# Kernel tuning notes

Hardware: AMD Instinct MI355X
Metric: run time of the kernel (lower is better)

The kernel has to match this reference:

```python
import jax, jax.numpy as jnp
import numpy as np
from jax import lax

PAD = 2          # shift_size // 2
SHIFT = 5        # shift_size


def _soft_shift(fp, gw, gb, axis):
    """fp: padded feature map [B,C,Hp,Wp]; gw: [S,C] 1x1-conv weight; gb: [S].
    Gated soft-shift along `axis` (2=H, 3=W), then crop padding."""
    logits = jnp.einsum('bchw,sc->bshw', fp, gw) + gb[None, :, None, None]
    w = jax.nn.softmax(logits, axis=1)  # [B,S,Hp,Wp]
    acc = jnp.zeros_like(fp)
    for i, s in enumerate(range(-PAD, PAD + 1)):
        acc = acc + jnp.roll(fp, s, axis=axis) * w[:, i:i + 1]
    return acc[:, :, PAD:-PAD, PAD:-PAD]


def _dwconv(x, w, b):
    # x: [B,C,H,W], w: [C,1,3,3] depthwise, b: [C]
    y = lax.conv_general_dilated(x, w, window_strides=(1, 1), padding='SAME',
                                 dimension_numbers=('NCHW', 'OIHW', 'NCHW'),
                                 feature_group_count=x.shape[1])
    return y + b[None, :, None, None]


def setup_inputs() -> dict:
    key = jax.random.key(0)
    ks = jax.random.split(key, 12)
    B, H, W = 16, 128, 128
    C, Ch = 96, 384
    x = jax.random.normal(ks[0], (B, H * W, C), dtype=jnp.float32)
    fc1_w = jax.random.normal(ks[1], (C, Ch), dtype=jnp.float32) * 0.02
    fc1_b = jnp.zeros((Ch,), dtype=jnp.float32)
    dw_w = jax.random.normal(ks[2], (Ch, 1, 3, 3), dtype=jnp.float32) * np.sqrt(2.0 / 9.0)
    dw_b = jnp.zeros((Ch,), dtype=jnp.float32)
    fc2_w = jax.random.normal(ks[3], (Ch, C), dtype=jnp.float32) * 0.02
    fc2_b = jnp.zeros((C,), dtype=jnp.float32)
    gh_w = jax.random.normal(ks[4], (SHIFT, C), dtype=jnp.float32) * np.sqrt(2.0 / SHIFT)
    gh_b = jnp.zeros((SHIFT,), dtype=jnp.float32)
    gw_w = jax.random.normal(ks[5], (SHIFT, Ch), dtype=jnp.float32) * np.sqrt(2.0 / SHIFT)
    gw_b = jnp.zeros((SHIFT,), dtype=jnp.float32)
    return {"x": x, "H": H, "W": W,
            "fc1_w": fc1_w, "fc1_b": fc1_b, "dw_w": dw_w, "dw_b": dw_b,
            "fc2_w": fc2_w, "fc2_b": fc2_b,
            "gh_w": gh_w, "gh_b": gh_b, "gw_w": gw_w, "gw_b": gw_b}


def reference(x, H, W, fc1_w, fc1_b, dw_w, dw_b, fc2_w, fc2_b, gh_w, gh_b, gw_w, gw_b):
    B, N, C = x.shape
    # soft-shift along H on input channels
    fmap = jnp.transpose(x, (0, 2, 1)).reshape(B, C, H, W)
    fmap_p = jnp.pad(fmap, ((0, 0), (0, 0), (PAD, PAD), (PAD, PAD)))
    mixed_h = _soft_shift(fmap_p, gh_w, gh_b, axis=2)          # [B,C,H,W]
    tokens = jnp.transpose(mixed_h.reshape(B, C, H * W), (0, 2, 1))
    tokens = tokens @ fc1_w + fc1_b                            # [B,N,Ch]
    Ch = tokens.shape[-1]
    t = jnp.transpose(tokens, (0, 2, 1)).reshape(B, Ch, H, W)
    t = _dwconv(t, dw_w, dw_b)
    tokens = jnp.transpose(t.reshape(B, Ch, H * W), (0, 2, 1))
    tokens = jax.nn.gelu(tokens, approximate=False)
    # soft-shift along W on hidden channels
    fmap2 = jnp.transpose(tokens, (0, 2, 1)).reshape(B, Ch, H, W)
    fmap2_p = jnp.pad(fmap2, ((0, 0), (0, 0), (PAD, PAD), (PAD, PAD)))
    mixed_w = _soft_shift(fmap2_p, gw_w, gw_b, axis=3)         # [B,Ch,H,W]
    tokens2 = jnp.transpose(mixed_w.reshape(B, Ch, H * W), (0, 2, 1))
    return tokens2 @ fc2_w + fc2_b                             # [B,N,C_out]
```

## Files before the change

kernel.cpp:

```cpp
#include <hip/hip_runtime.h>
#include <cstddef>

#define Cc 96
#define CH 384
#define Mtok 262144
#define Mi   16384

typedef unsigned short us8 __attribute__((ext_vector_type(8)));
typedef float f8 __attribute__((ext_vector_type(8)));
typedef short s8v __attribute__((ext_vector_type(8)));
typedef float f4v __attribute__((ext_vector_type(4)));

static __device__ __forceinline__ float b2f(unsigned short s){
  union { unsigned u; float f; } v; v.u = ((unsigned)s) << 16; return v.f;
}
static __device__ __forceinline__ unsigned short f2b(float f){
  union { float f; unsigned u; } v; v.f = f;
  unsigned r = v.u + 0x7fffu + ((v.u >> 16) & 1u);
  return (unsigned short)(r >> 16);
}

__global__ __launch_bounds__(64) void k_wprep(const float* __restrict__ dww,
    float* __restrict__ wt_t){
  int i = blockIdx.x*64 + threadIdx.x;
  if (i < 9*CH){
    int tap = i / CH, c = i - tap*CH;
    wt_t[i] = dww[c*9 + tap];
  }
}

__global__ __launch_bounds__(256) void k_wprep2(const float* __restrict__ fc2w,
    unsigned short* __restrict__ Bp){
  int i = blockIdx.x*256 + threadIdx.x;
  int j = i & 7;
  int t = i >> 3;
  int l = t & 63;
  int u = t >> 6;
  int ks = u % 12, nt = u / 12;
  int k   = ks*32 + (l>>4)*8 + j;
  int col = nt*16 + (l&15);
  Bp[i] = f2b(fc2w[(size_t)k*96 + col]);
}

__global__ __launch_bounds__(256) void k_wprep1(const float* __restrict__ fc1w,
    unsigned short* __restrict__ Bp1){
  int i = blockIdx.x*256 + threadIdx.x;
  int j = i & 7;
  int t = i >> 3;
  int l = t & 63;
  int u = t >> 6;
  int ks = u % 3, nt = u / 3;
  int k   = ks*32 + (l>>4)*8 + j;
  int col = nt*16 + (l&15);
  Bp1[i] = f2b(fc1w[(size_t)k*CH + col]);
}

__global__ __launch_bounds__(320) void k_fc1f(const float* __restrict__ x,
    const float* __restrict__ gh_w, const float* __restrict__ gh_b,
    const unsigned short* __restrict__ Bp1, const float* __restrict__ fc1b,
    unsigned short* __restrict__ hid, int base, int Mloc){
  __shared__ unsigned short A[80][100];
  __shared__ unsigned short Y[80][104];
  __shared__ float wh_s[80][5];
  const int tid = threadIdx.x;
  const int bid = (int)blockIdx.x;
  const int img  = bid >> 8;
  const int rem  = bid & 255;
  const int band = rem >> 5;
  const int colg = rem & 31;
  const int h0 = band*16;
  const int w0 = colg*4;
  const size_t lbase = (size_t)img*16384;

  {
    const int sr = tid>>2, sq = tid&3;
    const int r = sr>>2, cw = sr&3;
    const int h = h0 + r - 2;
    const bool valid = ((unsigned)h < 128u);
    float part[5] = {0.f,0.f,0.f,0.f,0.f};
    if (valid){
      const float* src = &x[((size_t)base + lbase + h*128 + w0 + cw)*Cc + sq*24];
      #pragma unroll
      for (int p=0;p<3;++p){
        float4 v0 = *(const float4*)&src[p*8];
        float4 v1 = *(const float4*)&src[p*8+4];
        us8 ov;
        ov[0]=f2b(v0.x); ov[1]=f2b(v0.y); ov[2]=f2b(v0.z); ov[3]=f2b(v0.w);
        ov[4]=f2b(v1.x); ov[5]=f2b(v1.y); ov[6]=f2b(v1.z); ov[7]=f2b(v1.w);
        *(us8*)&A[sr][sq*24 + p*8] = ov;
        #pragma unroll
        for (int s=0;s<5;++s){
          float4 g0 = *(const float4*)&gh_w[s*Cc + sq*24 + p*8];
          float4 g1 = *(const float4*)&gh_w[s*Cc + sq*24 + p*8 + 4];
          part[s]=fmaf(v0.x,g0.x,part[s]); part[s]=fmaf(v0.y,g0.y,part[s]);
          part[s]=fmaf(v0.z,g0.z,part[s]); part[s]=fmaf(v0.w,g0.w,part[s]);
          part[s]=fmaf(v1.x,g1.x,part[s]); part[s]=fmaf(v1.y,g1.y,part[s]);
          part[s]=fmaf(v1.z,g1.z,part[s]); part[s]=fmaf(v1.w,g1.w,part[s]);
        }
      }
    } else {
      us8 z = {0,0,0,0,0,0,0,0};
      #pragma unroll
      for (int p=0;p<3;++p) *(us8*)&A[sr][sq*24 + p*8] = z;
    }
    #pragma unroll
    for (int s=0;s<5;++s){
      float v = part[s];
      v += __shfl_xor(v, 1, 64);
      v += __shfl_xor(v, 2, 64);
      part[s] = v;
    }
    if (sq==0 && valid){
      float l[5];
      #pragma unroll
      for (int s=0;s<5;++s) l[s] = part[s] + gh_b[s];
      float mx = fmaxf(fmaxf(fmaxf(l[0],l[1]),fmaxf(l[2],l[3])),l[4]);
      float sum=0.f;
      #pragma unroll
      for (int s=0;s<5;++s){ l[s]=__expf(l[s]-mx); sum+=l[s]; }
      float inv=1.f/sum;
      #pragma unroll
      for (int s=0;s<5;++s) wh_s[sr][s] = l[s]*inv;
    }
  }
  __syncthreads();

  const int wv = tid>>6, l = tid&63;
  const int row16 = l&15, g = l>>4;
  const int tl = tid>>2, q = tid&3;
  const int it = (2 + (tl>>2))*4 + (tl&3);
  const int hh = h0 + (tl>>2);
  float swgt[5];
  unsigned short* o = nullptr;
  if (tid < 256){
    #pragma unroll
    for (int i=0;i<5;++i){
      int h2 = hh - (i-2);
      swgt[i] = ((unsigned)h2 < 128u) ? wh_s[it][i] : 0.f;
    }
    o = &hid[(lbase + hh*128 + w0 + (tl&3))*CH];
  }

  #pragma unroll 1
  for (int chunk=0;chunk<4;++chunk){
    f4v acc[6];
    #pragma unroll
    for (int j=0;j<6;++j) acc[j] = (f4v){0.f,0.f,0.f,0.f};
    #pragma unroll
    for (int ks=0;ks<3;++ks){
      s8v a = *(const s8v*)&A[wv*16 + row16][ks*32 + g*8];
      #pragma unroll
      for (int j=0;j<6;++j){
        s8v b = *(const s8v*)&Bp1[((size_t)((chunk*6+j)*3+ks)*64 + l)*8];
        acc[j] = __builtin_amdgcn_mfma_f32_16x16x32_bf16(a, b, acc[j], 0, 0, 0);
      }
    }
    __syncthreads();
    #pragma unroll
    for (int j=0;j<6;++j){
      #pragma unroll
      for (int r=0;r<4;++r){
        Y[wv*16 + g*4 + r][j*16 + row16] = f2b(acc[j][r]);
      }
    }
    __syncthreads();
    if (tid < 256){
      const int c0 = chunk*96 + q*24;
      float acc2[24];
      #pragma unroll
      for (int j=0;j<24;++j) acc2[j] = fc1b[c0+j];
      #pragma unroll
      for (int i=0;i<5;++i){
        if (swgt[i] != 0.f){
          const unsigned short* yr = &Y[it - 4*(i-2)][q*24];
          #pragma unroll
          for (int p=0;p<3;++p){
            us8 v = *(const us8*)&yr[p*8];
            #pragma unroll
            for (int j=0;j<8;++j) acc2[p*8+j] = fmaf(swgt[i], b2f(v[j]), acc2[p*8+j]);
          }
        }
      }
      #pragma unroll
      for (int p=0;p<3;++p){
        us8 ov;
        #pragma unroll
        for (int j=0;j<8;++j) ov[j] = f2b(acc2[p*8+j]);
        *(us8*)&o[c0 + p*8] = ov;
      }
    }
  }
}

__global__ __launch_bounds__(256) void k_dw(const unsigned short* __restrict__ hid,
    const float* __restrict__ wt_t, const float* __restrict__ dwb,
    const float* __restrict__ gww, const float* __restrict__ gwb,
    unsigned short* __restrict__ hid2, float* __restrict__ ww, int Mloc){
  const int tid = threadIdx.x;
  const int nwg = (int)gridDim.x;
  const int bid = (int)blockIdx.x;
  const int wg  = (bid & 7)*(nwg >> 3) + (bid >> 3);
  const int m0 = wg*64;
  const int p  = tid>>3, cg = tid&7;
  const int m  = m0 + 2*p;
  const int h = (m>>7)&127, w = m&127;
  bool hok[3];
  #pragma unroll
  for (int k=0;k<3;++k) hok[k] = ((unsigned)(h+k-1) < 128u);
  bool c0ok = (w > 0);
  bool c3ok = (w <= 125);

  float part0[5] = {0.f,0.f,0.f,0.f,0.f};
  float part1[5] = {0.f,0.f,0.f,0.f,0.f};
  #pragma unroll 1
  for (int cc=0;cc<6;++cc){
    const int c = cg*8 + cc*64;
    float acc0[8], acc1[8];
    {
      f8 bias = *(const f8*)&dwb[c];
      #pragma unroll
      for (int j=0;j<8;++j){ acc0[j] = bias[j]; acc1[j] = bias[j]; }
    }
    #pragma unroll
    for (int kh=0;kh<3;++kh){
      if (!hok[kh]) continue;
      us8 cv[4];
      {
        const unsigned short* rr = &hid[(size_t)(m + (kh-1)*128)*CH + c];
        us8 z = {0,0,0,0,0,0,0,0};
        cv[0] = c0ok ? *(const us8*)(rr - CH)   : z;
        cv[1] = *(const us8*)rr;
        cv[2] = *(const us8*)(rr + CH);
        cv[3] = c3ok ? *(const us8*)(rr + 2*CH) : z;
      }
      #pragma unroll
      for (int kw=0;kw<3;++kw){
        f8 wf = *(const f8*)&wt_t[(kh*3+kw)*CH + c];
        #pragma unroll
        for (int j=0;j<8;++j){
          acc0[j] = fmaf(b2f(cv[kw  ][j]), wf[j], acc0[j]);
          acc1[j] = fmaf(b2f(cv[kw+1][j]), wf[j], acc1[j]);
        }
      }
    }
    us8 ov0, ov1;
    float g0[8], g1[8];
    #pragma unroll
    for (int j=0;j<8;++j){
      float a0 = acc0[j];
      float t0 = __expf(-a0*(1.5957691216f + 0.0713548996f*a0*a0));
      g0[j] = a0*__builtin_amdgcn_rcpf(1.f + t0);
      ov0[j] = f2b(g0[j]);
      float a1 = acc1[j];
      float t1 = __expf(-a1*(1.5957691216f + 0.0713548996f*a1*a1));
      g1[j] = a1*__builtin_amdgcn_rcpf(1.f + t1);
      ov1[j] = f2b(g1[j]);
    }
    *(us8*)&hid2[(size_t)m*CH + c]     = ov0;
    *(us8*)&hid2[(size_t)(m+1)*CH + c] = ov1;
    #pragma unroll
    for (int s=0;s<5;++s){
      f8 gw = *(const f8*)&gww[s*CH + c];
      #pragma unroll
      for (int j=0;j<8;++j){
        part0[s] = fmaf(g0[j], gw[j], part0[s]);
        part1[s] = fmaf(g1[j], gw[j], part1[s]);
      }
    }
  }
  #pragma unroll
  for (int s=0;s<5;++s){
    float v0 = part0[s];
    v0 += __shfl_xor(v0, 1, 64);
    v0 += __shfl_xor(v0, 2, 64);
    v0 += __shfl_xor(v0, 4, 64);
    part0[s] = v0;
    float v1 = part1[s];
    v1 += __shfl_xor(v1, 1, 64);
    v1 += __shfl_xor(v1, 2, 64);
    v1 += __shfl_xor(v1, 4, 64);
    part1[s] = v1;
  }
  if (cg==0){
    float l0[5], l1[5];
    #pragma unroll
    for (int s=0;s<5;++s){ l0[s] = part0[s] + gwb[s]; l1[s] = part1[s] + gwb[s]; }
    float mx0 = fmaxf(fmaxf(fmaxf(l0[0],l0[1]),fmaxf(l0[2],l0[3])),l0[4]);
    float mx1 = fmaxf(fmaxf(fmaxf(l1[0],l1[1]),fmaxf(l1[2],l1[3])),l1[4]);
    float s0=0.f, s1=0.f;
    #pragma unroll
    for (int s=0;s<5;++s){
      l0[s]=__expf(l0[s]-mx0); s0+=l0[s];
      l1[s]=__expf(l1[s]-mx1); s1+=l1[s];
    }
    float i0 = 1.f/s0, i1 = 1.f/s1;
    #pragma unroll
    for (int s=0;s<5;++s){
      ww[(size_t)s*Mloc + m]     = l0[s]*i0;
      ww[(size_t)s*Mloc + m + 1] = l1[s]*i1;
    }
  }
}

__global__ __launch_bounds__(320) void k_fc2f(const unsigned short* __restrict__ hid2,
    const float* __restrict__ ww, const unsigned short* __restrict__ Bp,
    const float* __restrict__ fc2b, float* __restrict__ out,
    int base, int Mloc){
  __shared__ unsigned short A[80][100];
  __shared__ unsigned short Y[80][104];
  const int tid = threadIdx.x;
  const int m0 = (int)blockIdx.x*64;
  const int w0 = m0 & 127;
  const int rowbase = m0 - w0;

  const int wv = tid>>6, l = tid&63;
  const int row16 = l&15, g = l>>4;
  const int srow = tid>>2, ssq = tid&3;
  const int swtok = w0 - 2 + srow;
  const bool svalid = (srow < 68) && ((unsigned)swtok < 128u);
  const unsigned short* ssrc = svalid ?
      &hid2[(size_t)(rowbase + swtok)*CH + ssq*24] : nullptr;

  f4v acc[6];
  #pragma unroll
  for (int j=0;j<6;++j) acc[j] = (f4v){0.f,0.f,0.f,0.f};

  #pragma unroll 1
  for (int chunk=0;chunk<4;++chunk){
    if (svalid){
      #pragma unroll
      for (int p=0;p<3;++p)
        *(us8*)&A[srow][ssq*24 + p*8] = *(const us8*)&ssrc[chunk*96 + p*8];
    } else {
      us8 z = {0,0,0,0,0,0,0,0};
      #pragma unroll
      for (int p=0;p<3;++p) *(us8*)&A[srow][ssq*24 + p*8] = z;
    }
    __syncthreads();
    #pragma unroll
    for (int ks=0;ks<3;++ks){
      s8v a = *(const s8v*)&A[wv*16 + row16][ks*32 + g*8];
      #pragma unroll
      for (int nt=0;nt<6;++nt){
        s8v b = *(const s8v*)&Bp[((size_t)(nt*12 + chunk*3 + ks)*64 + l)*8];
        acc[nt] = __builtin_amdgcn_mfma_f32_16x16x32_bf16(a, b, acc[nt], 0, 0, 0);
      }
    }
    __syncthreads();
  }

  #pragma unroll
  for (int nt=0;nt<6;++nt){
    #pragma unroll
    for (int r=0;r<4;++r){
      Y[wv*16 + g*4 + r][nt*16 + row16] = f2b(acc[nt][r]);
    }
  }
  __syncthreads();

  if (tid < 256){
    const int t = tid>>2, q = tid&3;
    const int ml = m0 + t;
    const int gm = base + ml;
    const int wp = w0 + t;
    float swgt[5];
    #pragma unroll
    for (int i=0;i<5;++i){
      int w2 = wp - (i-2);
      swgt[i] = ((unsigned)w2 < 128u) ? ww[(size_t)i*Mloc + ml] : 0.f;
    }
    const int c0 = q*24;
    float acc2[24];
    #pragma unroll
    for (int j=0;j<24;++j) acc2[j] = fc2b[c0+j];
    #pragma unroll
    for (int i=0;i<5;++i){
      if (swgt[i] != 0.f){
        const unsigned short* yr = &Y[(t+2) - (i-2)][c0];
        #pragma unroll
        for (int p=0;p<3;++p){
          us8 v = *(const us8*)&yr[p*8];
          #pragma unroll
          for (int j=0;j<8;++j) acc2[p*8+j] = fmaf(swgt[i], b2f(v[j]), acc2[p*8+j]);
        }
      }
    }
    float* o = &out[(size_t)gm*96 + c0];
    #pragma unroll
    for (int p=0;p<6;++p)
      *(float4*)&o[p*4] = make_float4(acc2[p*4],acc2[p*4+1],acc2[p*4+2],acc2[p*4+3]);
  }
}

extern "C" void kernel_launch(void* const* d_in, const int* in_sizes, int n_in,
                              void* d_out, int out_size, void* d_ws, size_t ws_size,
                              hipStream_t stream) {
  const float* x     = (const float*)d_in[0];
  const float* fc1_w = (const float*)d_in[3];
  const float* fc1_b = (const float*)d_in[4];
  const float* dw_w  = (const float*)d_in[5];
  const float* dw_b  = (const float*)d_in[6];
  const float* fc2_w = (const float*)d_in[7];
  const float* fc2_b = (const float*)d_in[8];
  const float* gh_w  = (const float*)d_in[9];
  const float* gh_b  = (const float*)d_in[10];
  const float* gw_w  = (const float*)d_in[11];
  const float* gw_b  = (const float*)d_in[12];
  float* out = (float*)d_out;

  float* wt_t = (float*)d_ws;
  unsigned short* Bp  = (unsigned short*)((char*)d_ws + 13824);
  unsigned short* Bp1 = (unsigned short*)((char*)d_ws + 13824 + 73728);
  char*  wsc  = (char*)d_ws + 13824 + 73728 + 73728;
  size_t ws_rem = (ws_size > 161280) ? ws_size - 161280 : 0;

  k_wprep<<<(9*CH + 63)/64, 64, 0, stream>>>(dw_w, wt_t);
  k_wprep2<<<144, 256, 0, stream>>>(fc2_w, Bp);
  k_wprep1<<<144, 256, 0, stream>>>(fc1_w, Bp1);

  const size_t pi = (size_t)5*Mi*4 + (size_t)Mi*CH*2*2;
  int NI = (int)(ws_rem / pi);
  if (NI < 1) NI = 1;
  if (NI > 16) NI = 16;

  for (int b0 = 0; b0 < 16; b0 += NI) {
    int nb = (16 - b0 < NI) ? (16 - b0) : NI;
    int Mloc = nb * Mi;
    int base = b0 * Mi;
    float* ww = (float*)wsc;
    unsigned short* hid  = (unsigned short*)(ww + (size_t)5*Mloc);
    unsigned short* hid2 = hid + (size_t)Mloc*CH;
    k_fc1f<<<Mloc/64, 320, 0, stream>>>(x, gh_w, gh_b, Bp1, fc1_b, hid, base, Mloc);
    k_dw<<<Mloc/64, 256, 0, stream>>>(hid, wt_t, dw_b, gw_w, gw_b, hid2, ww, Mloc);
    k_fc2f<<<Mloc/64, 320, 0, stream>>>(hid2, ww, Bp, fc2_b, out, base, Mloc);
  }
}
```

Baseline: 497.7 us.

## Fuse depthwise conv, GELU and W-gate softmax into fc2 kernel

Merges the depthwise conv + GELU + gating-softmax kernel into the fc2 GEMM kernel, so each block computes the conv output for its 68-token halo window directly into shared memory. This drops the hid2 and gate-weight round trips through global memory and one kernel launch. In exchange, the 4 halo tokens per 64-token block get their conv recomputed, each thread now does 3x3 loads plus conv math inside the GEMM loop, and occupancy or latency hiding may suffer. Workspace needs shrink, so larger batch chunks fit per iteration.

```diff
diff --git a/kernel.cpp b/kernel.cpp
--- a/kernel.cpp
+++ b/kernel.cpp
@@ -192,145 +192,84 @@
   }
 }
 
-__global__ __launch_bounds__(256) void k_dw(const unsigned short* __restrict__ hid,
+__global__ __launch_bounds__(320) void k_dwfc2f(const unsigned short* __restrict__ hid,
     const float* __restrict__ wt_t, const float* __restrict__ dwb,
     const float* __restrict__ gww, const float* __restrict__ gwb,
-    unsigned short* __restrict__ hid2, float* __restrict__ ww, int Mloc){
-  const int tid = threadIdx.x;
-  const int nwg = (int)gridDim.x;
-  const int bid = (int)blockIdx.x;
-  const int wg  = (bid & 7)*(nwg >> 3) + (bid >> 3);
-  const int m0 = wg*64;
-  const int p  = tid>>3, cg = tid&7;
-  const int m  = m0 + 2*p;
-  const int h = (m>>7)&127, w = m&127;
-  bool hok[3];
-  #pragma unroll
-  for (int k=0;k<3;++k) hok[k] = ((unsigned)(h+k-1) < 128u);
-  bool c0ok = (w > 0);
-  bool c3ok = (w <= 125);
-
-  float part0[5] = {0.f,0.f,0.f,0.f,0.f};
-  float part1[5] = {0.f,0.f,0.f,0.f,0.f};
-  #pragma unroll 1
-  for (int cc=0;cc<6;++cc){
-    const int c = cg*8 + cc*64;
-    float acc0[8], acc1[8];
-    {
-      f8 bias = *(const f8*)&dwb[c];
-      #pragma unroll
-      for (int j=0;j<8;++j){ acc0[j] = bias[j]; acc1[j] = bias[j]; }
-    }
-    #pragma unroll
-    for (int kh=0;kh<3;++kh){
-      if (!hok[kh]) continue;
-      us8 cv[4];
-      {
-        const unsigned short* rr = &hid[(size_t)(m + (kh-1)*128)*CH + c];
-        us8 z = {0,0,0,0,0,0,0,0};
-        cv[0] = c0ok ? *(const us8*)(rr - CH)   : z;
-        cv[1] = *(const us8*)rr;
-        cv[2] = *(const us8*)(rr + CH);
-        cv[3] = c3ok ? *(const us8*)(rr + 2*CH) : z;
-      }
-      #pragma unroll
-      for (int kw=0;kw<3;++kw){
-        f8 wf = *(const f8*)&wt_t[(kh*3+kw)*CH + c];
-        #pragma unroll
-        for (int j=0;j<8;++j){
-          acc0[j] = fmaf(b2f(cv[kw  ][j]), wf[j], acc0[j]);
-          acc1[j] = fmaf(b2f(cv[kw+1][j]), wf[j], acc1[j]);
-        }
-      }
-    }
-    us8 ov0, ov1;
-    float g0[8], g1[8];
-    #pragma unroll
-    for (int j=0;j<8;++j){
-      float a0 = acc0[j];
-      float t0 = __expf(-a0*(1.5957691216f + 0.0713548996f*a0*a0));
-      g0[j] = a0*__builtin_amdgcn_rcpf(1.f + t0);
-      ov0[j] = f2b(g0[j]);
-      float a1 = acc1[j];
-      float t1 = __expf(-a1*(1.5957691216f + 0.0713548996f*a1*a1));
-      g1[j] = a1*__builtin_amdgcn_rcpf(1.f + t1);
-      ov1[j] = f2b(g1[j]);
-    }
-    *(us8*)&hid2[(size_t)m*CH + c]     = ov0;
-    *(us8*)&hid2[(size_t)(m+1)*CH + c] = ov1;
-    #pragma unroll
-    for (int s=0;s<5;++s){
-      f8 gw = *(const f8*)&gww[s*CH + c];
-      #pragma unroll
-      for (int j=0;j<8;++j){
-        part0[s] = fmaf(g0[j], gw[j], part0[s]);
-        part1[s] = fmaf(g1[j], gw[j], part1[s]);
-      }
-    }
-  }
-  #pragma unroll
-  for (int s=0;s<5;++s){
-    float v0 = part0[s];
-    v0 += __shfl_xor(v0, 1, 64);
-    v0 += __shfl_xor(v0, 2, 64);
-    v0 += __shfl_xor(v0, 4, 64);
-    part0[s] = v0;
-    float v1 = part1[s];
-    v1 += __shfl_xor(v1, 1, 64);
-    v1 += __shfl_xor(v1, 2, 64);
-    v1 += __shfl_xor(v1, 4, 64);
-    part1[s] = v1;
-  }
-  if (cg==0){
-    float l0[5], l1[5];
-    #pragma unroll
-    for (int s=0;s<5;++s){ l0[s] = part0[s] + gwb[s]; l1[s] = part1[s] + gwb[s]; }
-    float mx0 = fmaxf(fmaxf(fmaxf(l0[0],l0[1]),fmaxf(l0[2],l0[3])),l0[4]);
-    float mx1 = fmaxf(fmaxf(fmaxf(l1[0],l1[1]),fmaxf(l1[2],l1[3])),l1[4]);
-    float s0=0.f, s1=0.f;
-    #pragma unroll
-    for (int s=0;s<5;++s){
-      l0[s]=__expf(l0[s]-mx0); s0+=l0[s];
-      l1[s]=__expf(l1[s]-mx1); s1+=l1[s];
-    }
-    float i0 = 1.f/s0, i1 = 1.f/s1;
-    #pragma unroll
-    for (int s=0;s<5;++s){
-      ww[(size_t)s*Mloc + m]     = l0[s]*i0;
-      ww[(size_t)s*Mloc + m + 1] = l1[s]*i1;
-    }
-  }
-}
-
-__global__ __launch_bounds__(320) void k_fc2f(const unsigned short* __restrict__ hid2,
-    const float* __restrict__ ww, const unsigned short* __restrict__ Bp,
-    const float* __restrict__ fc2b, float* __restrict__ out,
-    int base, int Mloc){
+    const unsigned short* __restrict__ Bp, const float* __restrict__ fc2b,
+    float* __restrict__ out, int base, int Mloc){
   __shared__ unsigned short A[80][100];
   __shared__ unsigned short Y[80][104];
+  __shared__ float wgt_s[80][5];
   const int tid = threadIdx.x;
   const int m0 = (int)blockIdx.x*64;
   const int w0 = m0 & 127;
   const int rowbase = m0 - w0;
+  const int h = (m0>>7)&127;
+  bool hok[3];
+  #pragma unroll
+  for (int k=0;k<3;++k) hok[k] = ((unsigned)(h+k-1) < 128u);
+
+  const int srow = tid>>2, ssq = tid&3;
+  const int wt = w0 - 2 + srow;
+  const bool svalid = (srow < 68) && ((unsigned)wt < 128u);
+  const int tok = rowbase + (svalid ? wt : 0);
+  const bool wokm = svalid && (wt > 0);
+  const bool wokp = svalid && (wt < 127);
 
   const int wv = tid>>6, l = tid&63;
   const int row16 = l&15, g = l>>4;
-  const int srow = tid>>2, ssq = tid&3;
-  const int swtok = w0 - 2 + srow;
-  const bool svalid = (srow < 68) && ((unsigned)swtok < 128u);
-  const unsigned short* ssrc = svalid ?
-      &hid2[(size_t)(rowbase + swtok)*CH + ssq*24] : nullptr;
 
   f4v acc[6];
   #pragma unroll
   for (int j=0;j<6;++j) acc[j] = (f4v){0.f,0.f,0.f,0.f};
+  float part[5] = {0.f,0.f,0.f,0.f,0.f};
 
   #pragma unroll 1
   for (int chunk=0;chunk<4;++chunk){
     if (svalid){
       #pragma unroll
-      for (int p=0;p<3;++p)
-        *(us8*)&A[srow][ssq*24 + p*8] = *(const us8*)&ssrc[chunk*96 + p*8];
+      for (int p=0;p<3;++p){
+        const int c8 = chunk*96 + ssq*24 + p*8;
+        float a0[8];
+        {
+          f8 bias = *(const f8*)&dwb[c8];
+          #pragma unroll
+          for (int j=0;j<8;++j) a0[j] = bias[j];
+        }
+        #pragma unroll
+        for (int kh=0;kh<3;++kh){
+          if (!hok[kh]) continue;
+          const unsigned short* rr = &hid[(size_t)(tok + (kh-1)*128)*CH + c8];
+          us8 tv[3];
+          us8 z = {0,0,0,0,0,0,0,0};
+          tv[0] = wokm ? *(const us8*)(rr - CH) : z;
+          tv[1] = *(const us8*)rr;
+          tv[2] = wokp ? *(const us8*)(rr + CH) : z;
+          #pragma unroll
+          for (int kw=0;kw<3;++kw){
+            f8 wf = *(const f8*)&wt_t[(kh*3+kw)*CH + c8];
+            #pragma unroll
+            for (int j=0;j<8;++j)
+              a0[j] = fmaf(b2f(tv[kw][j]), wf[j], a0[j]);
+          }
+        }
+        us8 ov;
+        float gg[8];
+        #pragma unroll
+        for (int j=0;j<8;++j){
+          float a = a0[j];
+          float t = __expf(-a*(1.5957691216f + 0.0713548996f*a*a));
+          gg[j] = a*__builtin_amdgcn_rcpf(1.f + t);
+          ov[j] = f2b(gg[j]);
+        }
+        *(us8*)&A[srow][ssq*24 + p*8] = ov;
+        #pragma unroll
+        for (int s=0;s<5;++s){
+          f8 gw = *(const f8*)&gww[s*CH + c8];
+          #pragma unroll
+          for (int j=0;j<8;++j) part[s] = fmaf(gg[j], gw[j], part[s]);
+        }
+      }
     } else {
       us8 z = {0,0,0,0,0,0,0,0};
       #pragma unroll
@@ -355,6 +294,25 @@
     for (int r=0;r<4;++r){
       Y[wv*16 + g*4 + r][nt*16 + row16] = f2b(acc[nt][r]);
     }
+  }
+  #pragma unroll
+  for (int s=0;s<5;++s){
+    float v = part[s];
+    v += __shfl_xor(v, 1, 64);
+    v += __shfl_xor(v, 2, 64);
+    part[s] = v;
+  }
+  if (ssq==0 && svalid){
+    float lg[5];
+    #pragma unroll
+    for (int s=0;s<5;++s) lg[s] = part[s] + gwb[s];
+    float mx = fmaxf(fmaxf(fmaxf(lg[0],lg[1]),fmaxf(lg[2],lg[3])),lg[4]);
+    float sum=0.f;
+    #pragma unroll
+    for (int s=0;s<5;++s){ lg[s]=__expf(lg[s]-mx); sum+=lg[s]; }
+    float inv=1.f/sum;
+    #pragma unroll
+    for (int s=0;s<5;++s) wgt_s[srow][s] = lg[s]*inv;
   }
   __syncthreads();
 
@@ -367,7 +325,7 @@
     #pragma unroll
     for (int i=0;i<5;++i){
       int w2 = wp - (i-2);
-      swgt[i] = ((unsigned)w2 < 128u) ? ww[(size_t)i*Mloc + ml] : 0.f;
+      swgt[i] = ((unsigned)w2 < 128u) ? wgt_s[t+2][i] : 0.f;
     }
     const int c0 = q*24;
     float acc2[24];
@@ -418,7 +376,7 @@
   k_wprep2<<<144, 256, 0, stream>>>(fc2_w, Bp);
   k_wprep1<<<144, 256, 0, stream>>>(fc1_w, Bp1);
 
-  const size_t pi = (size_t)5*Mi*4 + (size_t)Mi*CH*2*2;
+  const size_t pi = (size_t)Mi*CH*2;
   int NI = (int)(ws_rem / pi);
   if (NI < 1) NI = 1;
   if (NI > 16) NI = 16;
@@ -427,11 +385,8 @@
     int nb = (16 - b0 < NI) ? (16 - b0) : NI;
     int Mloc = nb * Mi;
     int base = b0 * Mi;
-    float* ww = (float*)wsc;
-    unsigned short* hid  = (unsigned short*)(ww + (size_t)5*Mloc);
-    unsigned short* hid2 = hid + (size_t)Mloc*CH;
+    unsigned short* hid = (unsigned short*)wsc;
     k_fc1f<<<Mloc/64, 320, 0, stream>>>(x, gh_w, gh_b, Bp1, fc1_b, hid, base, Mloc);
-    k_dw<<<Mloc/64, 256, 0, stream>>>(hid, wt_t, dw_b, gw_w, gw_b, hid2, ww, Mloc);
-    k_fc2f<<<Mloc/64, 320, 0, stream>>>(hid2, ww, Bp, fc2_b, out, base, Mloc);
-  }
-}
+    k_dwfc2f<<<Mloc/64, 320, 0, stream>>>(hid, wt_t, dw_b, gw_w, gw_b, Bp, fc2_b, out, base, Mloc);
+  }
+}
```

Measured after the change: 725.9 us. 1.46x slower.
